# Optimization experiments

Hardware: AMD Instinct MI355X
Metric: run time of the kernel (lower is better)

## Reference

```python
import jax, jax.numpy as jnp
import numpy as np

HIDDEN = 1024
N_HEADS = 16
N_KV = 4
HEAD_DIM = HIDDEN // N_HEADS  # 64


def setup_inputs() -> dict:
    key = jax.random.key(0)
    ks = jax.random.split(key, 10)
    B, S, D = 2, 2048, HIDDEN
    s = 0.02
    return {
        "hidden_states": jax.random.normal(ks[0], (B, S, D), jnp.float32),
        "attention_mask": jnp.ones((B, S), jnp.float32),
        "Wq": jax.random.normal(ks[1], (D, N_HEADS * HEAD_DIM), jnp.float32) * s,
        "bq": jnp.zeros((N_HEADS * HEAD_DIM,), jnp.float32),
        "Wk": jax.random.normal(ks[2], (D, N_KV * HEAD_DIM), jnp.float32) * s,
        "bk": jnp.zeros((N_KV * HEAD_DIM,), jnp.float32),
        "Wv": jax.random.normal(ks[3], (D, N_KV * HEAD_DIM), jnp.float32) * s,
        "bv": jnp.zeros((N_KV * HEAD_DIM,), jnp.float32),
        "Wo": jax.random.normal(ks[4], (D, D), jnp.float32) * s,
        "bo": jnp.zeros((D,), jnp.float32),
    }


def _rope(x):
    # x: [B, H, S, Dh]; half-split RoPE as in the torch module
    S, Dh = x.shape[-2], x.shape[-1]
    inv_freq = 1.0 / (10000.0 ** (jnp.arange(0, Dh, 2, dtype=jnp.float32) / Dh))
    freqs = jnp.arange(S, dtype=jnp.float32)[:, None] * inv_freq[None, :]  # [S, Dh/2]
    cos, sin = jnp.cos(freqs), jnp.sin(freqs)
    x1, x2 = jnp.split(x, 2, axis=-1)
    return jnp.concatenate([x1 * cos - x2 * sin, x1 * sin + x2 * cos], axis=-1)


def reference(hidden_states, attention_mask, Wq, bq, Wk, bk, Wv, bv, Wo, bo):
    B, S, D = hidden_states.shape
    q = (hidden_states @ Wq + bq).reshape(B, S, N_HEADS, HEAD_DIM).transpose(0, 2, 1, 3)
    k = (hidden_states @ Wk + bk).reshape(B, S, N_KV, HEAD_DIM).transpose(0, 2, 1, 3)
    v = (hidden_states @ Wv + bv).reshape(B, S, N_KV, HEAD_DIM).transpose(0, 2, 1, 3)
    q = _rope(q)
    k = _rope(k)
    rep = N_HEADS // N_KV
    k = jnp.repeat(k, rep, axis=1)  # [B, H, S, Dh]
    v = jnp.repeat(v, rep, axis=1)
    bias = (1.0 - attention_mask[:, None, None, :]) * -1e9  # [B,1,1,S]
    scores = jnp.einsum("bhqd,bhkd->bhqk", q, k) / jnp.sqrt(jnp.float32(HEAD_DIM))
    attn = jax.nn.softmax(scores + bias, axis=-1)
    out = jnp.einsum("bhqk,bhkd->bhqd", attn, v)
    out = out.transpose(0, 2, 1, 3).reshape(B, S, D)
    return out @ Wo + bo
```

## Files before the change

### kernel.cpp

```cpp
#include <hip/hip_runtime.h>

typedef __bf16 bf16;
typedef __attribute__((ext_vector_type(8))) __bf16 bf16x8;
typedef __attribute__((ext_vector_type(4))) __bf16 bf16x4;
typedef __attribute__((ext_vector_type(4))) float f32x4;

#define LOG2E 1.44269504088896340736f
#define QSCALE 0.18033688011112042f

__device__ inline void tr_tile(const float* __restrict__ in, bf16* __restrict__ out,
                               int R, int C, int bx, int by, int tid) {
    __shared__ float t[32][33];
    int tx = tid & 31, ty = tid >> 5;
    int rbase = by * 32, cbase = bx * 32;
#pragma unroll
    for (int i = 0; i < 4; i++) {
        int r = ty + i * 8;
        t[r][tx] = in[(size_t)(rbase + r) * C + cbase + tx];
    }
    __syncthreads();
#pragma unroll
    for (int i = 0; i < 4; i++) {
        int r = ty + i * 8;
        out[(size_t)(cbase + r) * R + rbase + tx] = (bf16)t[tx][r];
    }
}

__global__ __launch_bounds__(256) void prep_k(const float* __restrict__ X,
                                              const float* __restrict__ Wq,
                                              const float* __restrict__ Wk,
                                              const float* __restrict__ Wv,
                                              const float* __restrict__ Wo,
                                              const float* __restrict__ mask,
                                              bf16* __restrict__ Xb,
                                              bf16* __restrict__ WqT,
                                              bf16* __restrict__ WkT,
                                              bf16* __restrict__ WvT,
                                              bf16* __restrict__ WoT,
                                              float2* __restrict__ rt,
                                              float* __restrict__ Mb,
                                              int* __restrict__ mflags) {
    int blk = blockIdx.x, tid = threadIdx.x;
    if (blk < 2048) {
        int idx = (blk * 256 + tid) * 8;
        float4 a = *(const float4*)(X + idx);
        float4 b = *(const float4*)(X + idx + 4);
        bf16 v[8] = {(bf16)a.x, (bf16)a.y, (bf16)a.z, (bf16)a.w,
                     (bf16)b.x, (bf16)b.y, (bf16)b.z, (bf16)b.w};
        *(uint4*)(Xb + idx) = *(const uint4*)v;
    } else if (blk < 3072) {
        int t = blk - 2048; tr_tile(Wq, WqT, 1024, 1024, t & 31, t >> 5, tid);
    } else if (blk < 3328) {
        int t = blk - 3072; tr_tile(Wk, WkT, 1024, 256, t & 7, t >> 3, tid);
    } else if (blk < 3584) {
        int t = blk - 3328; tr_tile(Wv, WvT, 1024, 256, t & 7, t >> 3, tid);
    } else if (blk < 4608) {
        int t = blk - 3584; tr_tile(Wo, WoT, 1024, 1024, t & 31, t >> 5, tid);
    } else if (blk < 4864) {
        int idx = (blk - 4608) * 256 + tid;
        int s = idx >> 5, i = idx & 31;
        float inv = exp2f(-0.41524100370589830f * (float)i);
        float ang = (float)s * inv;
        rt[idx] = make_float2(cosf(ang), sinf(ang));
    } else {
        __shared__ int sflag;
        int b = blk - 4864;
        if (tid == 0) sflag = 1;
        __syncthreads();
        const float* mrow = mask + (size_t)b * 2048;
        int i0 = tid * 8;
        bool ones = true;
#pragma unroll
        for (int j = 0; j < 8; j++) {
            float m = mrow[i0 + j];
            if (m != 1.0f) ones = false;
            Mb[(size_t)b * 2048 + i0 + j] = (1.0f - m) * (-1e9f) * LOG2E;
        }
        if (!ones) sflag = 0;
        __syncthreads();
        if (tid == 0) mflags[b] = sflag;
    }
}

__global__ __launch_bounds__(256) void vtrans_k(const unsigned short* __restrict__ in,
                                                unsigned short* __restrict__ out) {
    __shared__ unsigned short t[32][33];
    int z = blockIdx.z;
    const unsigned short* ip = in + (size_t)z * 2048 * 64;
    unsigned short* op = out + (size_t)z * 2048 * 64;
    int tx = threadIdx.x & 31, ty = threadIdx.x >> 5;
    int rbase = blockIdx.y * 32, cbase = blockIdx.x * 32;
#pragma unroll
    for (int i = 0; i < 4; i++) {
        int r = ty + i * 8;
        t[r][tx] = ip[(size_t)(rbase + r) * 64 + cbase + tx];
    }
    __syncthreads();
#pragma unroll
    for (int i = 0; i < 4; i++) {
        int r = ty + i * 8;
        op[(size_t)(cbase + r) * 2048 + rbase + tx] = t[tx][r];
    }
}

__device__ __forceinline__ void gemm_main_12864(const bf16* __restrict__ A,
                                                const bf16* __restrict__ BT,
                                                int m0, int n0, int tid,
                                                f32x4 (&acc)[2][4]) {
    __shared__ bf16 As[128 * 64];
    __shared__ bf16 Bs[64 * 64];
    int w = tid >> 6, lane = tid & 63, l15 = lane & 15, quad = lane >> 4;

    int srow = lane >> 3;
    int kx = ((lane & 7) ^ srow) * 8;
    const bf16* ga0 = A + (size_t)(m0 + w * 32 + srow) * 1024 + kx;
    const bf16* gb0 = BT + (size_t)(n0 + w * 16 + srow) * 1024 + kx;
    bf16* la0 = As + (w * 32) * 64 + lane * 8;
    bf16* lb0 = Bs + (w * 16) * 64 + lane * 8;

    for (int k0 = 0; k0 < 1024; k0 += 64) {
#pragma unroll
        for (int p = 0; p < 4; p++)
            __builtin_amdgcn_global_load_lds(
                (const __attribute__((address_space(1))) unsigned int*)(ga0 + (size_t)p * 8 * 1024 + k0),
                (__attribute__((address_space(3))) unsigned int*)(la0 + p * 512), 16, 0, 0);
#pragma unroll
        for (int p = 0; p < 2; p++)
            __builtin_amdgcn_global_load_lds(
                (const __attribute__((address_space(1))) unsigned int*)(gb0 + (size_t)p * 8 * 1024 + k0),
                (__attribute__((address_space(3))) unsigned int*)(lb0 + p * 512), 16, 0, 0);
        __syncthreads();
#pragma unroll
        for (int half = 0; half < 2; half++) {
            bf16x8 a[2], bfr[4];
            int kp = ((half * 4 + quad) ^ (l15 & 7)) * 8;
#pragma unroll
            for (int i = 0; i < 2; i++)
                a[i] = *(const bf16x8*)&As[(w * 32 + i * 16 + l15) * 64 + kp];
#pragma unroll
            for (int j = 0; j < 4; j++)
                bfr[j] = *(const bf16x8*)&Bs[(j * 16 + l15) * 64 + kp];
#pragma unroll
            for (int i = 0; i < 2; i++)
#pragma unroll
                for (int j = 0; j < 4; j++)
                    acc[i][j] = __builtin_amdgcn_mfma_f32_16x16x32_bf16(a[i], bfr[j], acc[i][j], 0, 0, 0);
        }
        __syncthreads();
    }
}

__global__ __launch_bounds__(256) void qkv_gemm2(const bf16* __restrict__ Xb,
                                                 const bf16* __restrict__ WTall,
                                                 const float* __restrict__ bq,
                                                 const float* __restrict__ bk,
                                                 const float* __restrict__ bv,
                                                 const float2* __restrict__ rt,
                                                 bf16* __restrict__ Qb,
                                                 bf16* __restrict__ Kb,
                                                 bf16* __restrict__ Vb) {
    int tt = blockIdx.x, gy = blockIdx.y, tid = threadIdx.x;
    f32x4 acc[2][4] = {};
    gemm_main_12864(Xb, WTall, tt * 128, gy * 64, tid, acc);

    int w = tid >> 6, lane = tid & 63, l15 = lane & 15, quad = lane >> 4;
    const float* bias;
    bf16* dst;
    int mode, head;
    if (gy < 16)      { head = gy;      bias = bq + head * 64; dst = Qb; mode = 0; }
    else if (gy < 20) { head = gy - 16; bias = bk + head * 64; dst = Kb; mode = 1; }
    else              { head = gy - 20; bias = bv + head * 64; dst = Vb; mode = 2; }

#pragma unroll
    for (int i = 0; i < 2; i++) {
#pragma unroll
        for (int r = 0; r < 4; r++) {
            int token = tt * 128 + w * 32 + i * 16 + quad * 4 + r;
            int b = token >> 11, s = token & 2047;
            float vals[4];
#pragma unroll
            for (int j = 0; j < 4; j++) vals[j] = acc[i][j][r] + bias[j * 16 + l15];
            if (mode <= 1) {
#pragma unroll
                for (int c = 0; c < 2; c++) {
                    float2 cs2 = rt[s * 32 + c * 16 + l15];
                    float x1 = vals[c], x2 = vals[c + 2];
                    vals[c]     = x1 * cs2.x - x2 * cs2.y;
                    vals[c + 2] = x1 * cs2.y + x2 * cs2.x;
                }
            }
            if (mode == 0) {
#pragma unroll
                for (int j = 0; j < 4; j++) vals[j] *= QSCALE;
            }
            size_t base;
            if (mode == 0) base = (((size_t)b * 16 + head) * 2048 + s) * 64;
            else           base = (((size_t)b * 4  + head) * 2048 + s) * 64;
#pragma unroll
            for (int j = 0; j < 4; j++) dst[base + j * 16 + l15] = (bf16)vals[j];
        }
    }
}

__global__ __launch_bounds__(256) void oproj_gemm2(const bf16* __restrict__ Ab,
                                                   const bf16* __restrict__ WoT,
                                                   const float* __restrict__ bo,
                                                   float* __restrict__ out) {
    int tt = blockIdx.x, nt = blockIdx.y, tid = threadIdx.x;
    f32x4 acc[2][4] = {};
    gemm_main_12864(Ab, WoT, tt * 128, nt * 64, tid, acc);

    int w = tid >> 6, lane = tid & 63, l15 = lane & 15, quad = lane >> 4;
#pragma unroll
    for (int i = 0; i < 2; i++) {
#pragma unroll
        for (int r = 0; r < 4; r++) {
            int token = tt * 128 + w * 32 + i * 16 + quad * 4 + r;
#pragma unroll
            for (int j = 0; j < 4; j++) {
                int n = nt * 64 + j * 16 + l15;
                out[(size_t)token * 1024 + n] = acc[i][j][r] + bo[n];
            }
        }
    }
}

__global__ __launch_bounds__(256) void attn_k(const bf16* __restrict__ Qb,
                                              const bf16* __restrict__ Kb,
                                              const bf16* __restrict__ VbT,
                                              const float* __restrict__ Mb,
                                              const int* __restrict__ mflags,
                                              bf16* __restrict__ Ob) {
    int qt = blockIdx.x, h = blockIdx.y, b = blockIdx.z;
    int kvh = h >> 2;

    __shared__ bf16 Ks[64 * 64];
    __shared__ bf16 Vs[64 * 64];
    __shared__ unsigned short Ps[4][32 * 72];

    int tid = threadIdx.x, w = tid >> 6, lane = tid & 63, l15 = lane & 15, quad = lane >> 4;

    const bool maskOnes = (mflags[b] != 0);

    bf16x8 qa[2][2];
#pragma unroll
    for (int g = 0; g < 2; g++) {
        size_t qbase = (((size_t)b * 16 + h) * 2048 + (size_t)qt * 128 + w * 32 + g * 16 + l15) * 64;
        qa[g][0] = *(const bf16x8*)(Qb + qbase + quad * 8);
        qa[g][1] = *(const bf16x8*)(Qb + qbase + 32 + quad * 8);
    }

    f32x4 oacc[2][4] = {};
    float lsum[2] = {0.f, 0.f};

    size_t kRow = ((size_t)b * 4 + kvh) * 2048;
    size_t vRow = ((size_t)b * 4 + kvh) * 64;
    const float* mrow = Mb + (size_t)b * 2048 + quad * 4;

    int srow = (lane >> 3);
    int kx = ((lane & 7) ^ srow) * 8;
    const bf16* gk0 = Kb + (kRow + w * 16 + srow) * 64 + kx;
    const bf16* gv0 = VbT + (vRow + w * 16 + srow) * 2048 + kx;
    bf16* lk0 = Ks + (w * 16) * 64 + lane * 8;
    bf16* lv0 = Vs + (w * 16) * 64 + lane * 8;

    for (int kt = 0; kt < 32; kt++) {
#pragma unroll
        for (int p = 0; p < 2; p++) {
            __builtin_amdgcn_global_load_lds(
                (const __attribute__((address_space(1))) unsigned int*)(gk0 + ((size_t)kt * 64 + p * 8) * 64),
                (__attribute__((address_space(3))) unsigned int*)(lk0 + p * 512), 16, 0, 0);
            __builtin_amdgcn_global_load_lds(
                (const __attribute__((address_space(1))) unsigned int*)(gv0 + (size_t)p * 8 * 2048 + kt * 64),
                (__attribute__((address_space(3))) unsigned int*)(lv0 + p * 512), 16, 0, 0);
        }
        __syncthreads();

        bf16x8 ka[4][2];
#pragma unroll
        for (int c = 0; c < 4; c++) {
            int row = c * 16 + l15;
#pragma unroll
            for (int half = 0; half < 2; half++) {
                int kp = ((half * 4 + quad) ^ (l15 & 7)) * 8;
                ka[c][half] = *(const bf16x8*)&Ks[row * 64 + kp];
            }
        }

        f32x4 sc[2][4];
#pragma unroll
        for (int g = 0; g < 2; g++)
#pragma unroll
            for (int c = 0; c < 4; c++) {
                f32x4 z = {};
                z = __builtin_amdgcn_mfma_f32_16x16x32_bf16(ka[c][0], qa[g][0], z, 0, 0, 0);
                z = __builtin_amdgcn_mfma_f32_16x16x32_bf16(ka[c][1], qa[g][1], z, 0, 0, 0);
                sc[g][c] = z;
            }
        if (!maskOnes) {
#pragma unroll
            for (int c = 0; c < 4; c++) {
                f32x4 bias4 = *(const f32x4*)(mrow + kt * 64 + c * 16);
#pragma unroll
                for (int r = 0; r < 4; r++) { sc[0][c][r] += bias4[r]; sc[1][c][r] += bias4[r]; }
            }
        }

#pragma unroll
        for (int g = 0; g < 2; g++) {
            float rs = 0.f;
#pragma unroll
            for (int c = 0; c < 4; c++)
#pragma unroll
                for (int r = 0; r < 4; r++) { sc[g][c][r] = exp2f(sc[g][c][r]); rs += sc[g][c][r]; }
            lsum[g] += rs;
#pragma unroll
            for (int c = 0; c < 4; c++) {
                bf16x4 pv = {(bf16)sc[g][c][0], (bf16)sc[g][c][1], (bf16)sc[g][c][2], (bf16)sc[g][c][3]};
                *(bf16x4*)&Ps[w][(g * 16 + l15) * 72 + c * 16 + quad * 4] = pv;
            }
        }

        bf16x8 vb[4][2];
#pragma unroll
        for (int c = 0; c < 4; c++) {
            int row = c * 16 + l15;
#pragma unroll
            for (int half = 0; half < 2; half++) {
                int kp = ((half * 4 + quad) ^ (l15 & 7)) * 8;
                vb[c][half] = *(const bf16x8*)&Vs[row * 64 + kp];
            }
        }
        bf16x8 pa[2][2];
#pragma unroll
        for (int g = 0; g < 2; g++) {
            pa[g][0] = *(const bf16x8*)&Ps[w][(g * 16 + l15) * 72 + quad * 8];
            pa[g][1] = *(const bf16x8*)&Ps[w][(g * 16 + l15) * 72 + 32 + quad * 8];
        }
#pragma unroll
        for (int g = 0; g < 2; g++)
#pragma unroll
            for (int c = 0; c < 4; c++) {
                oacc[g][c] = __builtin_amdgcn_mfma_f32_16x16x32_bf16(pa[g][0], vb[c][0], oacc[g][c], 0, 0, 0);
                oacc[g][c] = __builtin_amdgcn_mfma_f32_16x16x32_bf16(pa[g][1], vb[c][1], oacc[g][c], 0, 0, 0);
            }
        __syncthreads();
    }

#pragma unroll
    for (int g = 0; g < 2; g++) {
        lsum[g] += __shfl_xor(lsum[g], 16, 64);
        lsum[g] += __shfl_xor(lsum[g], 32, 64);
        float linv[4];
#pragma unroll
        for (int r = 0; r < 4; r++) linv[r] = 1.0f / __shfl(lsum[g], quad * 4 + r, 64);
#pragma unroll
        for (int r = 0; r < 4; r++) {
            int q = qt * 128 + w * 32 + g * 16 + quad * 4 + r;
            size_t base = ((size_t)b * 2048 + q) * 1024 + h * 64;
#pragma unroll
            for (int c = 0; c < 4; c++) Ob[base + c * 16 + l15] = (bf16)(oacc[g][c][r] * linv[r]);
        }
    }
}

extern "C" void kernel_launch(void* const* d_in, const int* in_sizes, int n_in,
                              void* d_out, int out_size, void* d_ws, size_t ws_size,
                              hipStream_t stream) {
    const float* X    = (const float*)d_in[0];
    const float* mask = (const float*)d_in[1];
    const float* Wq   = (const float*)d_in[2];
    const float* bq   = (const float*)d_in[3];
    const float* Wk   = (const float*)d_in[4];
    const float* bk   = (const float*)d_in[5];
    const float* Wv   = (const float*)d_in[6];
    const float* bv   = (const float*)d_in[7];
    const float* Wo   = (const float*)d_in[8];
    const float* bo   = (const float*)d_in[9];
    float* out = (float*)d_out;
    bf16* ws  = (bf16*)d_ws;

    bf16* Xb  = ws;
    bf16* WqT = Xb + (size_t)4096 * 1024;
    bf16* WkT = WqT + 1024 * 1024;
    bf16* WvT = WkT + 256 * 1024;
    bf16* WoT = WvT + 256 * 1024;
    bf16* Qb  = WoT + 1024 * 1024;
    bf16* Kb  = Qb + (size_t)2 * 16 * 2048 * 64;
    bf16* Vb  = Kb + (size_t)2 * 4 * 2048 * 64;
    bf16* Ab  = Vb + (size_t)2 * 4 * 2048 * 64;
    float2* rt = (float2*)(Ab + (size_t)2 * 2048 * 1024);
    float* Mb  = (float*)(rt + 2048 * 32);
    int* mflags = (int*)(Mb + 2 * 2048);
    bf16* VbT = Xb;

    prep_k<<<4866, 256, 0, stream>>>(X, Wq, Wk, Wv, Wo, mask, Xb, WqT, WkT, WvT, WoT, rt, Mb, mflags);
    qkv_gemm2<<<dim3(32, 24), 256, 0, stream>>>(Xb, WqT, bq, bk, bv, rt, Qb, Kb, Vb);
    vtrans_k<<<dim3(2, 64, 8), 256, 0, stream>>>((const unsigned short*)Vb, (unsigned short*)VbT);
    attn_k<<<dim3(16, 16, 2), 256, 0, stream>>>(Qb, Kb, VbT, Mb, mflags, Ab);
    oproj_gemm2<<<dim3(32, 16), 256, 0, stream>>>(Ab, WoT, bo, out);
}
```

Baseline: 199.9 us.

## Double-buffer K/V tiles in attention to prefetch the next tile during compute

The attention kernel now keeps two LDS buffers each for K and V. While the current tile is consumed, the async global-to-LDS loads for the next key tile are issued into the other buffer. The per-iteration barrier that waited right after the loads is gone, so load latency can overlap with the QK MFMAs, the softmax and the PV MFMAs. In exchange, K/V shared memory doubles, which may lower how many blocks fit per CU.

```diff
diff --git a/kernel.cpp b/kernel.cpp
--- a/kernel.cpp
+++ b/kernel.cpp
@@ -234,8 +234,8 @@
     int qt = blockIdx.x, h = blockIdx.y, b = blockIdx.z;
     int kvh = h >> 2;
 
-    __shared__ bf16 Ks[64 * 64];
-    __shared__ bf16 Vs[64 * 64];
+    __shared__ bf16 Ks[2][64 * 64];
+    __shared__ bf16 Vs[2][64 * 64];
     __shared__ unsigned short Ps[4][32 * 72];
 
     int tid = threadIdx.x, w = tid >> 6, lane = tid & 63, l15 = lane & 15, quad = lane >> 4;
@@ -261,20 +261,30 @@
     int kx = ((lane & 7) ^ srow) * 8;
     const bf16* gk0 = Kb + (kRow + w * 16 + srow) * 64 + kx;
     const bf16* gv0 = VbT + (vRow + w * 16 + srow) * 2048 + kx;
-    bf16* lk0 = Ks + (w * 16) * 64 + lane * 8;
-    bf16* lv0 = Vs + (w * 16) * 64 + lane * 8;
+    int lofs = (w * 16) * 64 + lane * 8;
+
+#define STAGE(KT, BUF)                                                                              \
+    do {                                                                                            \
+        _Pragma("unroll")                                                                           \
+        for (int p = 0; p < 2; p++) {                                                               \
+            __builtin_amdgcn_global_load_lds(                                                       \
+                (const __attribute__((address_space(1))) unsigned int*)(gk0 + ((size_t)(KT) * 64 + p * 8) * 64), \
+                (__attribute__((address_space(3))) unsigned int*)(&Ks[BUF][0] + lofs + p * 512), 16, 0, 0); \
+            __builtin_amdgcn_global_load_lds(                                                       \
+                (const __attribute__((address_space(1))) unsigned int*)(gv0 + (size_t)p * 8 * 2048 + (KT) * 64), \
+                (__attribute__((address_space(3))) unsigned int*)(&Vs[BUF][0] + lofs + p * 512), 16, 0, 0); \
+        }                                                                                           \
+    } while (0)
+
+    STAGE(0, 0);
+    __syncthreads();
 
     for (int kt = 0; kt < 32; kt++) {
-#pragma unroll
-        for (int p = 0; p < 2; p++) {
-            __builtin_amdgcn_global_load_lds(
-                (const __attribute__((address_space(1))) unsigned int*)(gk0 + ((size_t)kt * 64 + p * 8) * 64),
-                (__attribute__((address_space(3))) unsigned int*)(lk0 + p * 512), 16, 0, 0);
-            __builtin_amdgcn_global_load_lds(
-                (const __attribute__((address_space(1))) unsigned int*)(gv0 + (size_t)p * 8 * 2048 + kt * 64),
-                (__attribute__((address_space(3))) unsigned int*)(lv0 + p * 512), 16, 0, 0);
-        }
-        __syncthreads();
+        int cb = kt & 1;
+        if (kt < 31) STAGE(kt + 1, cb ^ 1);
+
+        const bf16* ksb = &Ks[cb][0];
+        const bf16* vsb = &Vs[cb][0];
 
         bf16x8 ka[4][2];
 #pragma unroll
@@ -283,7 +293,7 @@
 #pragma unroll
             for (int half = 0; half < 2; half++) {
                 int kp = ((half * 4 + quad) ^ (l15 & 7)) * 8;
-                ka[c][half] = *(const bf16x8*)&Ks[row * 64 + kp];
+                ka[c][half] = *(const bf16x8*)&ksb[row * 64 + kp];
             }
         }
 
@@ -328,7 +338,7 @@
 #pragma unroll
             for (int half = 0; half < 2; half++) {
                 int kp = ((half * 4 + quad) ^ (l15 & 7)) * 8;
-                vb[c][half] = *(const bf16x8*)&Vs[row * 64 + kp];
+                vb[c][half] = *(const bf16x8*)&vsb[row * 64 + kp];
             }
         }
         bf16x8 pa[2][2];
@@ -346,6 +356,7 @@
             }
         __syncthreads();
     }
+#undef STAGE
 
 #pragma unroll
     for (int g = 0; g < 2; g++) {
```

Result: no change. 196.5 us (-1.7%).
